# Kernel optimization log

Measured on AMD Instinct MI355X. Metric: run time of the kernel, lower is better.

Reference implementation:

```python
import jax, jax.numpy as jnp
import numpy as np

N = 50000
R = 8
E = 100000
D_IN = 768
D_H = 256
LN_EPS = 1e-5


def _layer_norm(h, g, b):
    mu = jnp.mean(h, axis=-1, keepdims=True)
    var = jnp.mean((h - mu) ** 2, axis=-1, keepdims=True)
    return (h - mu) * jax.lax.rsqrt(var + LN_EPS) * g + b


def _rgcn_layer(x, node_w, edge_src, edge_tgt, W_rel, W_self_w, W_self_b, ln_g, ln_b):
    # x: [N, d_in]; edge_src/edge_tgt: [R, E]; W_rel: [R, d_in, d_out]
    n = x.shape[0]
    out = x @ W_self_w + W_self_b  # self loop
    for r in range(W_rel.shape[0]):  # fixed, small relation count
        src = edge_src[r]
        tgt = edge_tgt[r]
        feats = x[src] * node_w[src][:, None]          # gather + nuclearity scale, [E, d_in]
        msg = feats @ W_rel[r]                          # per-relation linear, [E, d_out]
        agg = jax.ops.segment_sum(msg, tgt, num_segments=n)                 # scatter_add
        cnt = jax.ops.segment_sum(jnp.ones(src.shape[0], x.dtype), tgt, num_segments=n)
        out = out + agg / jnp.clip(cnt, 1.0)[:, None]  # mean over relation neighbors
    return _layer_norm(jax.nn.relu(out), ln_g, ln_b)   # dropout = identity (eval)


def setup_inputs() -> dict:
    key = jax.random.key(0)
    ks = jax.random.split(key, 10)
    x = jax.random.normal(ks[0], (N, D_IN), dtype=jnp.float32)
    node_weights = jax.random.uniform(ks[1], (N,), dtype=jnp.float32)
    edge_src = jax.random.randint(ks[2], (R, E), 0, N, dtype=jnp.int32)
    edge_tgt = jax.random.randint(ks[3], (R, E), 0, N, dtype=jnp.int32)
    W_rel0 = jax.random.normal(ks[4], (R, D_IN, D_H), dtype=jnp.float32) / np.sqrt(D_IN)
    W_self0_w = jax.random.normal(ks[5], (D_IN, D_H), dtype=jnp.float32) / np.sqrt(D_IN)
    W_self0_b = jnp.zeros((D_H,), jnp.float32)
    W_rel1 = jax.random.normal(ks[6], (R, D_H, D_H), dtype=jnp.float32) / np.sqrt(D_H)
    W_self1_w = jax.random.normal(ks[7], (D_H, D_H), dtype=jnp.float32) / np.sqrt(D_H)
    W_self1_b = jnp.zeros((D_H,), jnp.float32)
    ones = jnp.ones((D_H,), jnp.float32)
    zeros = jnp.zeros((D_H,), jnp.float32)
    return {
        "x": x, "node_weights": node_weights,
        "edge_src": edge_src, "edge_tgt": edge_tgt,
        "W_rel0": W_rel0, "W_self0_w": W_self0_w, "W_self0_b": W_self0_b,
        "ln0_g": ones, "ln0_b": zeros,
        "W_rel1": W_rel1, "W_self1_w": W_self1_w, "W_self1_b": W_self1_b,
        "ln1_g": ones, "ln1_b": zeros,
    }


def reference(x, node_weights, edge_src, edge_tgt,
              W_rel0, W_self0_w, W_self0_b, ln0_g, ln0_b,
              W_rel1, W_self1_w, W_self1_b, ln1_g, ln1_b):
    h = _rgcn_layer(x, node_weights, edge_src, edge_tgt,
                    W_rel0, W_self0_w, W_self0_b, ln0_g, ln0_b)
    h = _rgcn_layer(h, node_weights, edge_src, edge_tgt,
                    W_rel1, W_self1_w, W_self1_b, ln1_g, ln1_b)
    return h  # [N, 256]
```

## Files before the change

### kernel.cpp

```cpp
#include <hip/hip_runtime.h>
#include <stdint.h>

#define N_NODES 50000
#define M_PAD   50048
#define R_REL   8
#define E_EDGES 100000
#define D_IN    768
#define D_H     256
#define N_CAT   2304
#define LN_EPS  1e-5f

#define TILES_N 18
#define TILES_M 391
#define T_TOT   (TILES_N * TILES_M)
#define T_PER_XCD ((T_TOT + 7) / 8)
#define NCHUNK  49
#define EP_STRIDE 68
#define E_PAD_MAX 960000

typedef __attribute__((ext_vector_type(8))) __bf16        bf16x8;
typedef __attribute__((ext_vector_type(4))) float         f32x4;
typedef __attribute__((ext_vector_type(8))) unsigned short u16x8;
typedef __attribute__((ext_vector_type(4))) unsigned short u16x4;
typedef __attribute__((ext_vector_type(4))) int            i32x4;

__device__ __forceinline__ float bf2f(unsigned short u) {
  union { float f; uint32_t i; } c; c.i = ((uint32_t)u) << 16; return c.f;
}
__device__ __forceinline__ unsigned short f2bf(float f) {
  uint32_t x = __float_as_uint(f);
  uint32_t r = (x + 0x7fffu + ((x >> 16) & 1u)) >> 16;
  return (unsigned short)r;
}

__device__ __forceinline__ void gload_lds16(const void* g, uint32_t lds_off) {
  __builtin_amdgcn_global_load_lds(
      (const __attribute__((address_space(1))) void*)(uintptr_t)g,
      (__attribute__((address_space(3))) void*)(uintptr_t)lds_off, 16, 0, 0);
}

__global__ void k_deg(const int* __restrict__ tgt, int* __restrict__ deg) {
  int e = blockIdx.x * 256 + threadIdx.x;
  if (e >= R_REL * E_EDGES) return;
  int r = e / E_EDGES;
  atomicAdd(&deg[r * N_NODES + tgt[e]], 1);
}

__global__ void k_ndeg(const int* __restrict__ deg, int* __restrict__ pdeg) {
  int t = blockIdx.x * 256 + threadIdx.x;
  if (t >= N_NODES) return;
  int s = 0;
#pragma unroll
  for (int r = 0; r < R_REL; ++r) s += deg[r * N_NODES + t];
  pdeg[t] = (s + 3) & ~3;
}

__global__ __launch_bounds__(256)
void k_scan1(const int* __restrict__ deg, int* __restrict__ rowptr,
             int* __restrict__ bsum) {
  __shared__ int wtot[4];
  const int chunk = blockIdx.x, tid = threadIdx.x;
  const int wave = tid >> 6, lane = tid & 63;
  const int i0 = chunk * 1024 + tid * 4;
  int v0 = 0, v1 = 0, v2 = 0, v3 = 0;
  const int* d = deg;
  if (chunk != NCHUNK - 1) {
    i32x4 v = *(const i32x4*)(d + i0);
    v0 = v[0]; v1 = v[1]; v2 = v[2]; v3 = v[3];
  } else {
    if (i0 + 0 < N_NODES) v0 = d[i0 + 0];
    if (i0 + 1 < N_NODES) v1 = d[i0 + 1];
    if (i0 + 2 < N_NODES) v2 = d[i0 + 2];
    if (i0 + 3 < N_NODES) v3 = d[i0 + 3];
  }
  const int tsum = v0 + v1 + v2 + v3;
  int inc = tsum;
#pragma unroll
  for (int off = 1; off < 64; off <<= 1) {
    int t = __shfl_up(inc, off, 64);
    if (lane >= off) inc += t;
  }
  if (lane == 63) wtot[wave] = inc;
  __syncthreads();
  int woff = 0;
#pragma unroll
  for (int w = 0; w < 4; ++w) woff += (w < wave) ? wtot[w] : 0;
  int excl = woff + inc - tsum;
  int* rp = rowptr;
  if (i0 + 0 < N_NODES) rp[i0 + 0] = excl;
  if (i0 + 1 < N_NODES) rp[i0 + 1] = excl + v0;
  if (i0 + 2 < N_NODES) rp[i0 + 2] = excl + v0 + v1;
  if (i0 + 3 < N_NODES) rp[i0 + 3] = excl + v0 + v1 + v2;
  if (tid == 0) bsum[chunk] = wtot[0] + wtot[1] + wtot[2] + wtot[3];
}

__global__ __launch_bounds__(64)
void k_scan2(const int* __restrict__ bsum, int* __restrict__ chunkoff,
             int* __restrict__ rowptr) {
  const int lane = threadIdx.x & 63;
  int v = (lane < NCHUNK) ? bsum[lane] : 0;
  int inc = v;
#pragma unroll
  for (int off = 1; off < 64; off <<= 1) {
    int t = __shfl_up(inc, off, 64);
    if (lane >= off) inc += t;
  }
  if (lane < NCHUNK) chunkoff[lane] = inc - v;
  if (lane == NCHUNK - 1) rowptr[N_NODES] = inc;
}

__global__ __launch_bounds__(256)
void k_scan3(const int* __restrict__ chunkoff, int* __restrict__ rowptr) {
  const int chunk = blockIdx.x;
  if (chunk == 0) return;
  const int off = chunkoff[chunk];
  const int i0 = chunk * 1024 + threadIdx.x * 4;
#pragma unroll
  for (int j = 0; j < 4; ++j)
    if (i0 + j < N_NODES) rowptr[i0 + j] += off;
}

__global__ void k_prep(const int* __restrict__ nodeptr, int2* __restrict__ scN) {
  int t = blockIdx.x * 256 + threadIdx.x;
  if (t >= N_NODES) return;
  scN[t] = make_int2(nodeptr[t], nodeptr[t + 1] - nodeptr[t]);
}

__global__ void k_fill(const int* __restrict__ src, const int* __restrict__ tgt,
                       const float* __restrict__ nw, const int* __restrict__ nodeptr,
                       const int* __restrict__ deg, int* __restrict__ cursor,
                       int2* __restrict__ e2) {
  int e = blockIdx.x * 256 + threadIdx.x;
  if (e >= R_REL * E_EDGES) return;
  int r = e / E_EDGES;
  int t = tgt[e], s = src[e];
  int pos = atomicAdd(&cursor[t], 1);
  int slot = nodeptr[t] + pos;
  float w = nw[s] / (float)deg[r * N_NODES + t];
  e2[slot] = make_int2(s | (r << 16), __float_as_int(w));
}

__global__ void k_cvt_x(const float* __restrict__ x, unsigned short* __restrict__ xb) {
  const size_t i = ((size_t)blockIdx.x * 256 + threadIdx.x) * 4;
  if (i >= (size_t)N_NODES * D_IN) return;
  const f32x4 v = *(const f32x4*)(x + i);
  u16x4 o = { f2bf(v[0]), f2bf(v[1]), f2bf(v[2]), f2bf(v[3]) };
  *(u16x4*)(xb + i) = o;
}

__global__ void k_cvt_w(const float* __restrict__ Ws, const float* __restrict__ Wr,
                        unsigned short* __restrict__ Wt, int K) {
  int idx = blockIdx.x * 256 + threadIdx.x;
  if (idx >= N_CAT * K) return;
  int n = idx / K, k = idx - n * K;
  float v = (n < 256) ? Ws[k * 256 + n]
                      : Wr[(size_t)((n - 256) >> 8) * K * 256 + k * 256 + (n & 255)];
  Wt[idx] = f2bf(v);
}

__global__ __launch_bounds__(256, 2)
void k_gemm(const unsigned short* __restrict__ A, const unsigned short* __restrict__ Bt,
            unsigned short* __restrict__ C, int K) {
  const int tile = (blockIdx.x & 7) * T_PER_XCD + (blockIdx.x >> 3);
  if (tile >= T_TOT) return;
  const int tileM = (tile / TILES_N) * 128;
  const int tileN = (tile % TILES_N) * 128;

  __shared__ __align__(16) char smem[34816];
  const int tid  = threadIdx.x;
  const int wave = tid >> 6, lane = tid & 63;
  const int wm = (wave >> 1) * 64, wn = (wave & 1) * 64;

  f32x4 acc[4][4] = {};

  const int rl = lane >> 3, sl8 = lane & 7;
  const int cch = sl8 ^ rl;
  const int srow = wave * 8 + rl;
  const unsigned short* gA = A  + (size_t)(tileM + srow) * K + cch * 8;
  const unsigned short* gB = Bt + (size_t)(tileN + srow) * K + cch * 8;
  const uint32_t ldsA = (uint32_t)(uintptr_t)smem;
  const uint32_t ldsB = ldsA + 16384;
  const uint32_t lA0 = ldsA + (wave * 8) * 128;
  const uint32_t lB0 = ldsB + (wave * 8) * 128;

  const char* pAb = smem         + (wm + (lane & 15)) * 128;
  const char* pBb = smem + 16384 + (wn + (lane & 15)) * 128;
  const int fph = lane >> 4, x7 = lane & 7;

  const int nk = K >> 6;
  for (int kt = 0; kt < nk; ++kt) {
    const size_t koff = (size_t)kt * 64;
    __syncthreads();
#pragma unroll
    for (int j = 0; j < 4; ++j) {
      gload_lds16(gA + (size_t)j * 32 * K + koff, lA0 + j * 4096);
      gload_lds16(gB + (size_t)j * 32 * K + koff, lB0 + j * 4096);
    }
    __syncthreads();
#pragma unroll
    for (int kk = 0; kk < 2; ++kk) {
      const int sA = ((kk * 4 + fph) ^ x7) * 16;
      bf16x8 af[4], bfr[4];
#pragma unroll
      for (int i = 0; i < 4; ++i) af[i]  = *(const bf16x8*)(pAb + i * 2048 + sA);
#pragma unroll
      for (int j = 0; j < 4; ++j) bfr[j] = *(const bf16x8*)(pBb + j * 2048 + sA);
#pragma unroll
      for (int i = 0; i < 4; ++i)
#pragma unroll
        for (int j = 0; j < 4; ++j)
          acc[i][j] = __builtin_amdgcn_mfma_f32_16x16x32_bf16(af[i], bfr[j], acc[i][j], 0, 0, 0);
    }
  }

  __syncthreads();
  unsigned short* st = (unsigned short*)smem + wave * (64 * EP_STRIDE);
  const int rq = (lane >> 4) * 4, cq = lane & 15;
#pragma unroll
  for (int i = 0; i < 4; ++i)
#pragma unroll
    for (int j = 0; j < 4; ++j)
#pragma unroll
      for (int p = 0; p < 4; ++p)
        st[(i * 16 + rq + p) * EP_STRIDE + j * 16 + cq] = f2bf(acc[i][j][p]);
#pragma unroll
  for (int pass = 0; pass < 8; ++pass) {
    const int row = pass * 8 + (lane >> 3);
    const unsigned short* rp_ = st + row * EP_STRIDE + (lane & 7) * 8;
    u16x4 lo = *(const u16x4*)(rp_);
    u16x4 hi = *(const u16x4*)(rp_ + 4);
    u16x8 v = { lo[0], lo[1], lo[2], lo[3], hi[0], hi[1], hi[2], hi[3] };
    size_t off = (size_t)(tileM + wm + row) * N_CAT + tileN + wn + (lane & 7) * 8;
    *(u16x8*)(C + off) = v;
  }
}

template <int FINAL>
__global__ __launch_bounds__(256)
void k_gather_ln(const unsigned short* __restrict__ Y, const int2* __restrict__ scN,
                 const int2* __restrict__ e2, const float* __restrict__ bias,
                 const float* __restrict__ g, const float* __restrict__ bln,
                 void* __restrict__ out) {
  const int wave = threadIdx.x >> 6, lane = threadIdx.x & 63;
  const int t = blockIdx.x * 4 + wave;
  if (t >= N_NODES) return;
  const int c0 = lane * 4;

  float a0, a1, a2, a3;
  {
    u16x4 sv = *(const u16x4*)(Y + (size_t)t * N_CAT + c0);
    f32x4 bb = *(const f32x4*)(bias + c0);
    a0 = bf2f(sv[0]) + bb[0];
    a1 = bf2f(sv[1]) + bb[1];
    a2 = bf2f(sv[2]) + bb[2];
    a3 = bf2f(sv[3]) + bb[3];
  }

  const int2 s = scN[t];
  const int2* ep = e2 + s.x;
  for (int idx = 0; idx < s.y; idx += 4) {
    const int2 p0 = ep[idx + 0];
    const int2 p1 = ep[idx + 1];
    const int2 p2 = ep[idx + 2];
    const int2 p3 = ep[idx + 3];
    const unsigned short* y0 = Y + (size_t)(p0.x & 0xFFFF) * N_CAT + (((p0.x >> 16) + 1) << 8) + c0;
    const unsigned short* y1 = Y + (size_t)(p1.x & 0xFFFF) * N_CAT + (((p1.x >> 16) + 1) << 8) + c0;
    const unsigned short* y2 = Y + (size_t)(p2.x & 0xFFFF) * N_CAT + (((p2.x >> 16) + 1) << 8) + c0;
    const unsigned short* y3 = Y + (size_t)(p3.x & 0xFFFF) * N_CAT + (((p3.x >> 16) + 1) << 8) + c0;
    u16x4 v0 = *(const u16x4*)y0;
    u16x4 v1 = *(const u16x4*)y1;
    u16x4 v2 = *(const u16x4*)y2;
    u16x4 v3 = *(const u16x4*)y3;
    const float w0 = __int_as_float(p0.y), w1 = __int_as_float(p1.y);
    const float w2 = __int_as_float(p2.y), w3 = __int_as_float(p3.y);
    a0 += w0 * bf2f(v0[0]) + w1 * bf2f(v1[0]) + w2 * bf2f(v2[0]) + w3 * bf2f(v3[0]);
    a1 += w0 * bf2f(v0[1]) + w1 * bf2f(v1[1]) + w2 * bf2f(v2[1]) + w3 * bf2f(v3[1]);
    a2 += w0 * bf2f(v0[2]) + w1 * bf2f(v1[2]) + w2 * bf2f(v2[2]) + w3 * bf2f(v3[2]);
    a3 += w0 * bf2f(v0[3]) + w1 * bf2f(v1[3]) + w2 * bf2f(v2[3]) + w3 * bf2f(v3[3]);
  }

  a0 = fmaxf(a0, 0.f); a1 = fmaxf(a1, 0.f); a2 = fmaxf(a2, 0.f); a3 = fmaxf(a3, 0.f);

  float s1 = (a0 + a1) + (a2 + a3);
#pragma unroll
  for (int off = 32; off > 0; off >>= 1) s1 += __shfl_xor(s1, off, 64);
  const float mu = s1 * (1.f / 256.f);
  const float d0 = a0 - mu, d1 = a1 - mu, d2 = a2 - mu, d3 = a3 - mu;
  float s2 = (d0 * d0 + d1 * d1) + (d2 * d2 + d3 * d3);
#pragma unroll
  for (int off = 32; off > 0; off >>= 1) s2 += __shfl_xor(s2, off, 64);
  const float rs = rsqrtf(s2 * (1.f / 256.f) + LN_EPS);

  f32x4 gg = *(const f32x4*)(g + c0);
  f32x4 ll = *(const f32x4*)(bln + c0);
  const float o0 = d0 * rs * gg[0] + ll[0];
  const float o1 = d1 * rs * gg[1] + ll[1];
  const float o2 = d2 * rs * gg[2] + ll[2];
  const float o3 = d3 * rs * gg[3] + ll[3];
  if (FINAL) {
    f32x4 o = { o0, o1, o2, o3 };
    *(f32x4*)((float*)out + (size_t)t * 256 + c0) = o;
  } else {
    u16x4 o = { f2bf(o0), f2bf(o1), f2bf(o2), f2bf(o3) };
    *(u16x4*)((unsigned short*)out + (size_t)t * 256 + c0) = o;
  }
}

extern "C" void kernel_launch(void* const* d_in, const int* in_sizes, int n_in,
                              void* d_out, int out_size, void* d_ws, size_t ws_size,
                              hipStream_t stream) {
  (void)in_sizes; (void)n_in; (void)out_size; (void)ws_size;
  const float* x   = (const float*)d_in[0];
  const float* nw  = (const float*)d_in[1];
  const int*   esrc = (const int*)d_in[2];
  const int*   etgt = (const int*)d_in[3];
  const float* Wr0 = (const float*)d_in[4];
  const float* Ws0 = (const float*)d_in[5];
  const float* Wb0 = (const float*)d_in[6];
  const float* g0  = (const float*)d_in[7];
  const float* b0  = (const float*)d_in[8];
  const float* Wr1 = (const float*)d_in[9];
  const float* Ws1 = (const float*)d_in[10];
  const float* Wb1 = (const float*)d_in[11];
  const float* g1  = (const float*)d_in[12];
  const float* b1  = (const float*)d_in[13];

  char* p = (char*)d_ws;
  auto carve = [&](size_t bytes) {
    char* q = p;
    p += (bytes + 511) & ~(size_t)511;
    return q;
  };
  unsigned short* Y   = (unsigned short*)carve((size_t)M_PAD * N_CAT * 2);
  unsigned short* xb  = (unsigned short*)carve((size_t)M_PAD * D_IN * 2);
  unsigned short* h   = (unsigned short*)carve((size_t)M_PAD * D_H * 2);
  unsigned short* Wt0 = (unsigned short*)carve((size_t)N_CAT * D_IN * 2);
  unsigned short* Wt1 = (unsigned short*)carve((size_t)N_CAT * D_H * 2);
  int*   deg     = (int*)carve((size_t)R_REL * N_NODES * 4);
  int*   pdeg    = (int*)carve((size_t)N_NODES * 4);
  int*   cursor  = (int*)carve((size_t)N_NODES * 4);
  int*   nodeptr = (int*)carve((size_t)(N_NODES + 1) * 4);
  int*   bsum    = (int*)carve((size_t)NCHUNK * 4);
  int*   chunkoff= (int*)carve((size_t)NCHUNK * 4);
  int2*  e2      = (int2*)carve((size_t)E_PAD_MAX * 8);
  int2*  scN     = (int2*)carve((size_t)N_NODES * 8);

  hipMemsetAsync(deg, 0, (size_t)R_REL * N_NODES * 4, stream);
  hipMemsetAsync(cursor, 0, (size_t)N_NODES * 4, stream);
  hipMemsetAsync(e2, 0, (size_t)E_PAD_MAX * 8, stream);
  k_deg<<<(R_REL * E_EDGES + 255) / 256, 256, 0, stream>>>(etgt, deg);
  k_ndeg<<<(N_NODES + 255) / 256, 256, 0, stream>>>(deg, pdeg);
  k_scan1<<<NCHUNK, 256, 0, stream>>>(pdeg, nodeptr, bsum);
  k_scan2<<<1, 64, 0, stream>>>(bsum, chunkoff, nodeptr);
  k_scan3<<<NCHUNK, 256, 0, stream>>>(chunkoff, nodeptr);
  k_prep<<<(N_NODES + 255) / 256, 256, 0, stream>>>(nodeptr, scN);
  k_fill<<<(R_REL * E_EDGES + 255) / 256, 256, 0, stream>>>(esrc, etgt, nw, nodeptr,
                                                            deg, cursor, e2);
  k_cvt_x<<<(N_NODES * D_IN / 4 + 255) / 256, 256, 0, stream>>>(x, xb);
  k_cvt_w<<<(N_CAT * D_IN + 255) / 256, 256, 0, stream>>>(Ws0, Wr0, Wt0, D_IN);
  k_cvt_w<<<(N_CAT * D_H + 255) / 256, 256, 0, stream>>>(Ws1, Wr1, Wt1, D_H);

  const int nblk = 8 * T_PER_XCD;
  k_gemm<<<nblk, 256, 0, stream>>>(xb, Wt0, Y, D_IN);
  k_gather_ln<0><<<N_NODES / 4, 256, 0, stream>>>(Y, scN, e2, Wb0, g0, b0, h);
  k_gemm<<<nblk, 256, 0, stream>>>(h, Wt1, Y, D_H);
  k_gather_ln<1><<<N_NODES / 4, 256, 0, stream>>>(Y, scN, e2, Wb1, g1, b1, d_out);
}
```

Before: 797.8 us.

## Reorder layer-1 to aggregate-then-transform with per-relation neighbor sums and K-concat GEMM

Layer 1 now gathers neighbor features per (node, relation) into an [N, 8*256] buffer first. It then runs a single GEMM with K=2304 (self plus 8 relations) producing 256 outputs, instead of projecting every node to 2304 outputs and gathering those. The edge list is bucketed per relation via per-(node, relation) cursors and offsets, and the GEMM epilogue switches to an XOR-swizzled LDS staging layout. This cuts the layer-1 output GEMM width and gather traffic, at the cost of an extra gather pass that writes a large intermediate and an extra LN kernel.

```diff
diff --git a/kernel.cpp b/kernel.cpp
--- a/kernel.cpp
+++ b/kernel.cpp
@@ -8,14 +8,11 @@
 #define D_IN    768
 #define D_H     256
 #define N_CAT   2304
+#define K1      2304
 #define LN_EPS  1e-5f
 
-#define TILES_N 18
 #define TILES_M 391
-#define T_TOT   (TILES_N * TILES_M)
-#define T_PER_XCD ((T_TOT + 7) / 8)
 #define NCHUNK  49
-#define EP_STRIDE 68
 #define E_PAD_MAX 960000
 
 typedef __attribute__((ext_vector_type(8))) __bf16        bf16x8;
@@ -126,16 +123,26 @@
   scN[t] = make_int2(nodeptr[t], nodeptr[t + 1] - nodeptr[t]);
 }
 
+__global__ void k_prep8(const int* __restrict__ nodeptr, const int* __restrict__ deg,
+                        int2* __restrict__ sc8) {
+  int id = blockIdx.x * 256 + threadIdx.x;
+  if (id >= N_NODES * 8) return;
+  int t = id >> 3, r = id & 7;
+  int base = nodeptr[t];
+  for (int rr = 0; rr < r; ++rr) base += deg[rr * N_NODES + t];
+  sc8[id] = make_int2(base, deg[r * N_NODES + t]);
+}
+
 __global__ void k_fill(const int* __restrict__ src, const int* __restrict__ tgt,
-                       const float* __restrict__ nw, const int* __restrict__ nodeptr,
-                       const int* __restrict__ deg, int* __restrict__ cursor,
+                       const float* __restrict__ nw, const int2* __restrict__ sc8,
+                       const int* __restrict__ deg, int* __restrict__ cursor8,
                        int2* __restrict__ e2) {
   int e = blockIdx.x * 256 + threadIdx.x;
   if (e >= R_REL * E_EDGES) return;
   int r = e / E_EDGES;
   int t = tgt[e], s = src[e];
-  int pos = atomicAdd(&cursor[t], 1);
-  int slot = nodeptr[t] + pos;
+  int pos = atomicAdd(&cursor8[t * 8 + r], 1);
+  int slot = sc8[t * 8 + r].x + pos;
   float w = nw[s] / (float)deg[r * N_NODES + t];
   e2[slot] = make_int2(s | (r << 16), __float_as_int(w));
 }
@@ -158,15 +165,29 @@
   Wt[idx] = f2bf(v);
 }
 
+__global__ void k_cvt_w1(const float* __restrict__ Ws, const float* __restrict__ Wr,
+                         unsigned short* __restrict__ Wt) {
+  int idx = blockIdx.x * 256 + threadIdx.x;
+  if (idx >= 256 * K1) return;
+  int n = idx / K1, k = idx - n * K1;
+  float v = (k < 256) ? Ws[k * 256 + n]
+                      : Wr[(size_t)(((k >> 8) - 1) * 256 + (k & 255)) * 256 + n];
+  Wt[idx] = f2bf(v);
+}
+
+#define EP_STORE(st, row, col, val) \
+  (st)[(row) * 64 + ((((col) >> 3) ^ ((row) & 7)) << 3) + ((col) & 7)] = (val)
+
 __global__ __launch_bounds__(256, 2)
 void k_gemm(const unsigned short* __restrict__ A, const unsigned short* __restrict__ Bt,
             unsigned short* __restrict__ C, int K) {
-  const int tile = (blockIdx.x & 7) * T_PER_XCD + (blockIdx.x >> 3);
-  if (tile >= T_TOT) return;
-  const int tileM = (tile / TILES_N) * 128;
-  const int tileN = (tile % TILES_N) * 128;
-
-  __shared__ __align__(16) char smem[34816];
+  const int TN = 18, TTOT = TN * TILES_M, TPX = (TTOT + 7) / 8;
+  const int tile = (blockIdx.x & 7) * TPX + (blockIdx.x >> 3);
+  if (tile >= TTOT) return;
+  const int tileM = (tile / TN) * 128;
+  const int tileN = (tile % TN) * 128;
+
+  __shared__ __align__(16) char smem[32768];
   const int tid  = threadIdx.x;
   const int wave = tid >> 6, lane = tid & 63;
   const int wm = (wave >> 1) * 64, wn = (wave & 1) * 64;
@@ -214,7 +235,7 @@
   }
 
   __syncthreads();
-  unsigned short* st = (unsigned short*)smem + wave * (64 * EP_STRIDE);
+  unsigned short* st = (unsigned short*)smem + wave * 4096;
   const int rq = (lane >> 4) * 4, cq = lane & 15;
 #pragma unroll
   for (int i = 0; i < 4; ++i)
@@ -222,25 +243,99 @@
     for (int j = 0; j < 4; ++j)
 #pragma unroll
       for (int p = 0; p < 4; ++p)
-        st[(i * 16 + rq + p) * EP_STRIDE + j * 16 + cq] = f2bf(acc[i][j][p]);
+        EP_STORE(st, i * 16 + rq + p, j * 16 + cq, f2bf(acc[i][j][p]));
 #pragma unroll
   for (int pass = 0; pass < 8; ++pass) {
     const int row = pass * 8 + (lane >> 3);
-    const unsigned short* rp_ = st + row * EP_STRIDE + (lane & 7) * 8;
-    u16x4 lo = *(const u16x4*)(rp_);
-    u16x4 hi = *(const u16x4*)(rp_ + 4);
-    u16x8 v = { lo[0], lo[1], lo[2], lo[3], hi[0], hi[1], hi[2], hi[3] };
+    u16x8 v = *(const u16x8*)(st + row * 64 + (((lane & 7) ^ (row & 7)) << 3));
     size_t off = (size_t)(tileM + wm + row) * N_CAT + tileN + wn + (lane & 7) * 8;
     *(u16x8*)(C + off) = v;
   }
 }
 
-template <int FINAL>
+__global__ __launch_bounds__(256, 2)
+void k_gemm2(const unsigned short* __restrict__ h, const unsigned short* __restrict__ G8,
+             const unsigned short* __restrict__ Bt, unsigned short* __restrict__ C) {
+  const int TTOT = 2 * TILES_M, TPX = (TTOT + 7) / 8;
+  const int tile = (blockIdx.x & 7) * TPX + (blockIdx.x >> 3);
+  if (tile >= TTOT) return;
+  const int tileM = (tile >> 1) * 128;
+  const int tileN = (tile & 1) * 128;
+
+  __shared__ __align__(16) char smem[32768];
+  const int tid  = threadIdx.x;
+  const int wave = tid >> 6, lane = tid & 63;
+  const int wm = (wave >> 1) * 64, wn = (wave & 1) * 64;
+
+  f32x4 acc[4][4] = {};
+
+  const int rl = lane >> 3, sl8 = lane & 7;
+  const int cch = sl8 ^ rl;
+  const int srow = wave * 8 + rl;
+  const unsigned short* gH = h  + (size_t)(tileM + srow) * 256  + cch * 8;
+  const unsigned short* gG = G8 + (size_t)(tileM + srow) * 2048 + cch * 8;
+  const unsigned short* gB = Bt + (size_t)(tileN + srow) * K1   + cch * 8;
+  const uint32_t ldsA = (uint32_t)(uintptr_t)smem;
+  const uint32_t ldsB = ldsA + 16384;
+  const uint32_t lA0 = ldsA + (wave * 8) * 128;
+  const uint32_t lB0 = ldsB + (wave * 8) * 128;
+
+  const char* pAb = smem         + (wm + (lane & 15)) * 128;
+  const char* pBb = smem + 16384 + (wn + (lane & 15)) * 128;
+  const int fph = lane >> 4, x7 = lane & 7;
+
+  for (int kt = 0; kt < (K1 >> 6); ++kt) {
+    const int koff = kt * 64;
+    const bool fromH = (kt < 4);
+    const unsigned short* a0 = fromH ? gH + koff : gG + (koff - 256);
+    const size_t astep = fromH ? (size_t)32 * 256 : (size_t)32 * 2048;
+    __syncthreads();
+#pragma unroll
+    for (int j = 0; j < 4; ++j) {
+      gload_lds16(a0 + (size_t)j * astep, lA0 + j * 4096);
+      gload_lds16(gB + (size_t)j * 32 * K1 + koff, lB0 + j * 4096);
+    }
+    __syncthreads();
+#pragma unroll
+    for (int kk = 0; kk < 2; ++kk) {
+      const int sA = ((kk * 4 + fph) ^ x7) * 16;
+      bf16x8 af[4], bfr[4];
+#pragma unroll
+      for (int i = 0; i < 4; ++i) af[i]  = *(const bf16x8*)(pAb + i * 2048 + sA);
+#pragma unroll
+      for (int j = 0; j < 4; ++j) bfr[j] = *(const bf16x8*)(pBb + j * 2048 + sA);
+#pragma unroll
+      for (int i = 0; i < 4; ++i)
+#pragma unroll
+        for (int j = 0; j < 4; ++j)
+          acc[i][j] = __builtin_amdgcn_mfma_f32_16x16x32_bf16(af[i], bfr[j], acc[i][j], 0, 0, 0);
+    }
+  }
+
+  __syncthreads();
+  unsigned short* st = (unsigned short*)smem + wave * 4096;
+  const int rq = (lane >> 4) * 4, cq = lane & 15;
+#pragma unroll
+  for (int i = 0; i < 4; ++i)
+#pragma unroll
+    for (int j = 0; j < 4; ++j)
+#pragma unroll
+      for (int p = 0; p < 4; ++p)
+        EP_STORE(st, i * 16 + rq + p, j * 16 + cq, f2bf(acc[i][j][p]));
+#pragma unroll
+  for (int pass = 0; pass < 8; ++pass) {
+    const int row = pass * 8 + (lane >> 3);
+    u16x8 v = *(const u16x8*)(st + row * 64 + (((lane & 7) ^ (row & 7)) << 3));
+    size_t off = (size_t)(tileM + wm + row) * 256 + tileN + wn + (lane & 7) * 8;
+    *(u16x8*)(C + off) = v;
+  }
+}
+
 __global__ __launch_bounds__(256)
-void k_gather_ln(const unsigned short* __restrict__ Y, const int2* __restrict__ scN,
-                 const int2* __restrict__ e2, const float* __restrict__ bias,
-                 const float* __restrict__ g, const float* __restrict__ bln,
-                 void* __restrict__ out) {
+void k_gather0(const unsigned short* __restrict__ Y, const int2* __restrict__ scN,
+               const int2* __restrict__ e2, const float* __restrict__ bias,
+               const float* __restrict__ g, const float* __restrict__ bln,
+               unsigned short* __restrict__ out) {
   const int wave = threadIdx.x >> 6, lane = threadIdx.x & 63;
   const int t = blockIdx.x * 4 + wave;
   if (t >= N_NODES) return;
@@ -293,17 +388,60 @@
 
   f32x4 gg = *(const f32x4*)(g + c0);
   f32x4 ll = *(const f32x4*)(bln + c0);
-  const float o0 = d0 * rs * gg[0] + ll[0];
-  const float o1 = d1 * rs * gg[1] + ll[1];
-  const float o2 = d2 * rs * gg[2] + ll[2];
-  const float o3 = d3 * rs * gg[3] + ll[3];
-  if (FINAL) {
-    f32x4 o = { o0, o1, o2, o3 };
-    *(f32x4*)((float*)out + (size_t)t * 256 + c0) = o;
-  } else {
-    u16x4 o = { f2bf(o0), f2bf(o1), f2bf(o2), f2bf(o3) };
-    *(u16x4*)((unsigned short*)out + (size_t)t * 256 + c0) = o;
-  }
+  u16x4 o = { f2bf(d0 * rs * gg[0] + ll[0]), f2bf(d1 * rs * gg[1] + ll[1]),
+              f2bf(d2 * rs * gg[2] + ll[2]), f2bf(d3 * rs * gg[3] + ll[3]) };
+  *(u16x4*)(out + (size_t)t * 256 + c0) = o;
+}
+
+__global__ __launch_bounds__(256)
+void k_gatherG(const unsigned short* __restrict__ h, const int2* __restrict__ sc8,
+               const int2* __restrict__ e2, unsigned short* __restrict__ G8) {
+  const int wave = threadIdx.x >> 6, lane = threadIdx.x & 63;
+  const int id = blockIdx.x * 4 + wave;
+  if (id >= N_NODES * 8) return;
+  const int t = id >> 3, r = id & 7;
+  const int c0 = lane * 4;
+  const int2 s = sc8[id];
+  float a0 = 0, a1 = 0, a2 = 0, a3 = 0;
+  for (int i = 0; i < s.y; ++i) {
+    const int2 p = e2[s.x + i];
+    const float w = __int_as_float(p.y);
+    u16x4 v = *(const u16x4*)(h + (size_t)(p.x & 0xFFFF) * 256 + c0);
+    a0 += w * bf2f(v[0]); a1 += w * bf2f(v[1]);
+    a2 += w * bf2f(v[2]); a3 += w * bf2f(v[3]);
+  }
+  u16x4 o = { f2bf(a0), f2bf(a1), f2bf(a2), f2bf(a3) };
+  *(u16x4*)(G8 + (size_t)t * 2048 + r * 256 + c0) = o;
+}
+
+__global__ __launch_bounds__(256)
+void k_ln(const unsigned short* __restrict__ Ypre, const float* __restrict__ bias,
+          const float* __restrict__ g, const float* __restrict__ bln,
+          float* __restrict__ out) {
+  const int wave = threadIdx.x >> 6, lane = threadIdx.x & 63;
+  const int t = blockIdx.x * 4 + wave;
+  if (t >= N_NODES) return;
+  const int c0 = lane * 4;
+  u16x4 sv = *(const u16x4*)(Ypre + (size_t)t * 256 + c0);
+  f32x4 bb = *(const f32x4*)(bias + c0);
+  float a0 = fmaxf(bf2f(sv[0]) + bb[0], 0.f);
+  float a1 = fmaxf(bf2f(sv[1]) + bb[1], 0.f);
+  float a2 = fmaxf(bf2f(sv[2]) + bb[2], 0.f);
+  float a3 = fmaxf(bf2f(sv[3]) + bb[3], 0.f);
+  float s1 = (a0 + a1) + (a2 + a3);
+#pragma unroll
+  for (int off = 32; off > 0; off >>= 1) s1 += __shfl_xor(s1, off, 64);
+  const float mu = s1 * (1.f / 256.f);
+  const float d0 = a0 - mu, d1 = a1 - mu, d2 = a2 - mu, d3 = a3 - mu;
+  float s2 = (d0 * d0 + d1 * d1) + (d2 * d2 + d3 * d3);
+#pragma unroll
+  for (int off = 32; off > 0; off >>= 1) s2 += __shfl_xor(s2, off, 64);
+  const float rs = rsqrtf(s2 * (1.f / 256.f) + LN_EPS);
+  f32x4 gg = *(const f32x4*)(g + c0);
+  f32x4 ll = *(const f32x4*)(bln + c0);
+  f32x4 o = { d0 * rs * gg[0] + ll[0], d1 * rs * gg[1] + ll[1],
+              d2 * rs * gg[2] + ll[2], d3 * rs * gg[3] + ll[3] };
+  *(f32x4*)(out + (size_t)t * 256 + c0) = o;
 }
 
 extern "C" void kernel_launch(void* const* d_in, const int* in_sizes, int n_in,
@@ -331,22 +469,25 @@
     p += (bytes + 511) & ~(size_t)511;
     return q;
   };
-  unsigned short* Y   = (unsigned short*)carve((size_t)M_PAD * N_CAT * 2);
-  unsigned short* xb  = (unsigned short*)carve((size_t)M_PAD * D_IN * 2);
-  unsigned short* h   = (unsigned short*)carve((size_t)M_PAD * D_H * 2);
-  unsigned short* Wt0 = (unsigned short*)carve((size_t)N_CAT * D_IN * 2);
-  unsigned short* Wt1 = (unsigned short*)carve((size_t)N_CAT * D_H * 2);
+  unsigned short* Y    = (unsigned short*)carve((size_t)M_PAD * N_CAT * 2);
+  unsigned short* G8   = Y;
+  unsigned short* xb   = (unsigned short*)carve((size_t)M_PAD * D_IN * 2);
+  unsigned short* h    = (unsigned short*)carve((size_t)M_PAD * 256 * 2);
+  unsigned short* Ypre = (unsigned short*)carve((size_t)M_PAD * 256 * 2);
+  unsigned short* Wt0  = (unsigned short*)carve((size_t)N_CAT * D_IN * 2);
+  unsigned short* Wt1b = (unsigned short*)carve((size_t)256 * K1 * 2);
   int*   deg     = (int*)carve((size_t)R_REL * N_NODES * 4);
   int*   pdeg    = (int*)carve((size_t)N_NODES * 4);
-  int*   cursor  = (int*)carve((size_t)N_NODES * 4);
+  int*   cursor8 = (int*)carve((size_t)N_NODES * 8 * 4);
   int*   nodeptr = (int*)carve((size_t)(N_NODES + 1) * 4);
   int*   bsum    = (int*)carve((size_t)NCHUNK * 4);
   int*   chunkoff= (int*)carve((size_t)NCHUNK * 4);
   int2*  e2      = (int2*)carve((size_t)E_PAD_MAX * 8);
   int2*  scN     = (int2*)carve((size_t)N_NODES * 8);
+  int2*  sc8     = (int2*)carve((size_t)N_NODES * 8 * 8);
 
   hipMemsetAsync(deg, 0, (size_t)R_REL * N_NODES * 4, stream);
-  hipMemsetAsync(cursor, 0, (size_t)N_NODES * 4, stream);
+  hipMemsetAsync(cursor8, 0, (size_t)N_NODES * 8 * 4, stream);
   hipMemsetAsync(e2, 0, (size_t)E_PAD_MAX * 8, stream);
   k_deg<<<(R_REL * E_EDGES + 255) / 256, 256, 0, stream>>>(etgt, deg);
   k_ndeg<<<(N_NODES + 255) / 256, 256, 0, stream>>>(deg, pdeg);
@@ -354,15 +495,16 @@
   k_scan2<<<1, 64, 0, stream>>>(bsum, chunkoff, nodeptr);
   k_scan3<<<NCHUNK, 256, 0, stream>>>(chunkoff, nodeptr);
   k_prep<<<(N_NODES + 255) / 256, 256, 0, stream>>>(nodeptr, scN);
-  k_fill<<<(R_REL * E_EDGES + 255) / 256, 256, 0, stream>>>(esrc, etgt, nw, nodeptr,
-                                                            deg, cursor, e2);
+  k_prep8<<<(N_NODES * 8 + 255) / 256, 256, 0, stream>>>(nodeptr, deg, sc8);
+  k_fill<<<(R_REL * E_EDGES + 255) / 256, 256, 0, stream>>>(esrc, etgt, nw, sc8,
+                                                            deg, cursor8, e2);
   k_cvt_x<<<(N_NODES * D_IN / 4 + 255) / 256, 256, 0, stream>>>(x, xb);
   k_cvt_w<<<(N_CAT * D_IN + 255) / 256, 256, 0, stream>>>(Ws0, Wr0, Wt0, D_IN);
-  k_cvt_w<<<(N_CAT * D_H + 255) / 256, 256, 0, stream>>>(Ws1, Wr1, Wt1, D_H);
-
-  const int nblk = 8 * T_PER_XCD;
-  k_gemm<<<nblk, 256, 0, stream>>>(xb, Wt0, Y, D_IN);
-  k_gather_ln<0><<<N_NODES / 4, 256, 0, stream>>>(Y, scN, e2, Wb0, g0, b0, h);
-  k_gemm<<<nblk, 256, 0, stream>>>(h, Wt1, Y, D_H);
-  k_gather_ln<1><<<N_NODES / 4, 256, 0, stream>>>(Y, scN, e2, Wb1, g1, b1, d_out);
-}
+  k_cvt_w1<<<(256 * K1 + 255) / 256, 256, 0, stream>>>(Ws1, Wr1, Wt1b);
+
+  k_gemm<<<8 * ((18 * TILES_M + 7) / 8), 256, 0, stream>>>(xb, Wt0, Y, D_IN);
+  k_gather0<<<(N_NODES + 3) / 4, 256, 0, stream>>>(Y, scN, e2, Wb0, g0, b0, h);
+  k_gatherG<<<(N_NODES * 8 + 3) / 4, 256, 0, stream>>>(h, sc8, e2, G8);
+  k_gemm2<<<8 * ((2 * TILES_M + 7) / 8), 256, 0, stream>>>(h, G8, Wt1b, Ypre);
+  k_ln<<<(N_NODES + 3) / 4, 256, 0, stream>>>(Ypre, Wb1, g1, b1, (float*)d_out);
+}
```

Result: slower. 916.6 us (+14.9%).
